# Performance work log

Hardware: AMD Instinct MI355X
Metric: run time of the kernel (lower is better)

The kernel has to match this reference:

```python
import math
import jax, jax.numpy as jnp
import numpy as np
from jax.scipy.linalg import cho_factor, cho_solve, block_diag

NUM_SENSORS = 64
T_STEPS = 2048
LOG2PI = float(np.log(2.0 * np.pi))

NCV_PROCESS_NOISE = np.array([[1.0/3.0, 0.0, 0.5, 0.0],
                              [0.0, 1.0/3.0, 0.0, 0.5],
                              [0.5, 0.0, 1.0, 0.0],
                              [0.0, 0.5, 0.0, 1.0]], dtype=np.float32)
NCV_TRANSITION_MATRIX = np.array([[1.0, 0.0, 1.0, 0.0],
                                  [0.0, 1.0, 0.0, 1.0],
                                  [0.0, 0.0, 1.0, 0.0],
                                  [0.0, 0.0, 0.0, 1.0]], dtype=np.float32)


def setup_inputs() -> dict:
    key = jax.random.key(0)
    k1, k2 = jax.random.split(key)
    track = jax.random.normal(k1, (T_STEPS, 2), dtype=jnp.float32)
    # positive covariance scales for the bias prior (torch param init ~ ones)
    bias_scales = jax.random.uniform(k2, (2,), jnp.float32, 0.5, 1.5)
    obs_noise = jnp.float32(0.7)
    trans_noise = jnp.float32(0.3)
    return {"track": track, "bias_scales": bias_scales,
            "obs_noise": obs_noise, "trans_noise": trans_noise}


def _hmm_forward(track, bias_scales, obs_noise, trans_noise, num_sensors):
    S = num_sensors
    OD = 2 * S           # obs_dim
    D = OD + 4           # augmented latent: [bias(OD); state(4)]
    T = track.shape[0]
    dt = track.dtype

    # observation matrix exactly as in torch source:
    # eye(4,2).expand(S,4,2).transpose(0,-1).reshape(4, OD)
    E = jnp.eye(4, 2, dtype=dt)
    Hobs = jnp.transpose(jnp.broadcast_to(E, (S, 4, 2)), (2, 1, 0)).reshape(4, OD)
    # augmented emission: y = bias + state @ Hobs  ->  H_aug z
    Haug = jnp.concatenate([jnp.eye(OD, dtype=dt), Hobs.T], axis=1)  # (OD, D)

    F = jnp.asarray(NCV_TRANSITION_MATRIX, dt)
    # trans scale_tril = trans_noise * chol(NCV_Q) -> cov = trans_noise^2 * NCV_Q
    Qs = (trans_noise ** 2) * jnp.asarray(NCV_PROCESS_NOISE, dt)
    A = block_diag(jnp.eye(OD, dtype=dt), F)                         # (D, D)
    Q = block_diag(jnp.zeros((OD, OD), dt), Qs)                      # (D, D)
    # obs scale_tril = obs_noise * I -> cov = obs_noise^2 * I
    R = (obs_noise ** 2) * jnp.eye(OD, dtype=dt)

    # bias prior covariance = diag(bias_scales interleaved per sensor)
    bias_var = jnp.broadcast_to(bias_scales, (S, 2)).reshape(-1)     # (OD,)
    m0 = jnp.zeros((D,), dt)
    P0 = jnp.diag(jnp.concatenate([bias_var, jnp.ones((4,), dt)]))

    # obs vector per step: x.expand(S,2).reshape(-1) (interleaved repeat)
    ys = jnp.broadcast_to(track[:, None, :], (T, S, 2)).reshape(T, OD)

    def step(carry, y):
        m, P, ll = carry
        # predict
        mp = A @ m
        Pp = A @ P @ A.T + Q
        # innovation
        HP = Haug @ Pp                      # (OD, D)
        Sm = HP @ Haug.T + R                # (OD, OD)
        cf = cho_factor(Sm, lower=True)
        v = y - Haug @ mp                   # (OD,)
        # update
        K = cho_solve(cf, HP)               # S^{-1} H Pp, (OD, D)
        m_new = mp + K.T @ v
        P_new = Pp - HP.T @ K
        P_new = 0.5 * (P_new + P_new.T)
        # log-likelihood of innovation
        logdet = 2.0 * jnp.sum(jnp.log(jnp.diag(cf[0])))
        quad = v @ cho_solve(cf, v)
        ll = ll - 0.5 * (OD * LOG2PI + logdet + quad)
        return (m_new, P_new, ll), None

    (mT, PT, ll), _ = jax.lax.scan(step, (m0, P0, jnp.zeros((), dt)), ys)
    # funsor's remaining Gaussian over (bias, state_T) has precision = inv(filtered cov)
    cfP = cho_factor(PT, lower=True)
    prec = cho_solve(cfP, jnp.eye(D, dtype=dt))
    return ll, prec


def reference(track, bias_scales, obs_noise, trans_noise):
    return _hmm_forward(track, bias_scales, obs_noise, trans_noise, NUM_SENSORS)
```

## Files before the change

### kernel.cpp

```cpp
#include <hip/hip_runtime.h>
#include <math.h>

#define L2PI 1.8378770664093454835606594728112
#define LN2  0.69314718055994530941723212145818
#define MAGIC 0x7E57C0DE

struct LP {
    float jFF, jFL, jFB, jLL, jLB, jBB;
    float hF, hL, hB, g, dm, de;
};

struct Cn { float qa, qb, qc, wa, wb, ri, Cstep; };

__device__ __forceinline__ float shf(float v, int s) { return __shfl(v, s, 64); }
__device__ __forceinline__ float sx (float v, int m) { return __shfl_xor(v, m, 64); }

__device__ __forceinline__ LP init_lane(float x0, float x1, const Cn& C, int i, int j) {
    LP P;
    float v = 0.0f;
    if (i == j) v = (i < 2) ? C.qa : C.qc;
    if ((i ^ j) == 2) v = C.wa;
    P.jFF = v;
    v = 0.0f;
    if (j == (i & 1))     v = (i < 2) ? -C.qa : -C.wa;
    if (j == (i & 1) + 2) v = (i < 2) ? -C.qb : -C.wb;
    P.jFL = v;
    P.jFB = 0.0f;
    v = 0.0f;
    if (i == j) v = ((i < 2) ? C.qa : C.qc) + (((i & 1) == 0) ? 2.0f*C.ri : 0.0f);
    if ((i ^ j) == 2) v = C.qb;
    P.jLL = v;
    P.jLB = (((i == 0) && (j < 2)) || ((i == 2) && (j >= 2))) ? C.ri : 0.0f;
    P.jBB = (i == j) ? C.ri : 0.0f;
    P.hF = 0.0f;
    P.hL = ((j & 1) == 0) ? C.ri * (x0 + x1) : 0.0f;
    P.hB = C.ri * ((j & 1) ? x1 : x0);
    P.g  = -C.ri * (x0*x0 + x1*x1) + C.Cstep;
    P.dm = 1.0f; P.de = 0.0f;
    return P;
}

__device__ __forceinline__ LP compose(const LP& P1, const LP& P2, int gb, int i, int j) {
    float hm = P1.hL + P2.hF;
    float Mb = P1.jLB + P2.jFB;
    float S  = P1.jLL + P2.jFF;
    float dm = P1.dm * P2.dm;
    float de = P1.de + P2.de;
    { int ex; dm = frexpf(dm, &ex); de += (float)ex; }
    const int r0 = (j == 0) ? 1 : 0;
    const int r1 = (j <= 1) ? 2 : 1;
    const int r2 = (j <= 2) ? 3 : 2;
    const int c0 = (i == 0) ? 1 : 0;
    const int c1 = (i <= 1) ? 2 : 1;
    const int c2 = (i <= 2) ? 3 : 2;
    float m00 = shf(S, gb + 4*r0 + c0), m01 = shf(S, gb + 4*r0 + c1), m02 = shf(S, gb + 4*r0 + c2);
    float m10 = shf(S, gb + 4*r1 + c0), m11 = shf(S, gb + 4*r1 + c1), m12 = shf(S, gb + 4*r1 + c2);
    float m20 = shf(S, gb + 4*r2 + c0), m21 = shf(S, gb + 4*r2 + c1), m22 = shf(S, gb + 4*r2 + c2);
    float d0 = fmaf(m11, m22, -m12*m21);
    float d1 = fmaf(m10, m22, -m12*m20);
    float d2 = fmaf(m10, m21, -m11*m20);
    float det3 = m00*d0 - m01*d1 + m02*d2;
    float adj = (((i + j) & 1) ? -det3 : det3);
    float sji = shf(S, gb + 4*j + i);
    float t = sji * adj;
    t += sx(t, 4); t += sx(t, 8);
    float det = t;
    dm *= det; { int ex; dm = frexpf(dm, &ex); de += (float)ex; }
    const float Si = adj * (1.0f / det);
    float sr[4], sc[4], f1r[4], f1T[4], f2c[4], f2T[4], mc[4], mT[4], hmc[4];
    #pragma unroll
    for (int r = 0; r < 4; ++r) {
        sr[r]  = shf(Si, gb + 4*i + r);
        sc[r]  = shf(Si, gb + 4*r + j);
        f1r[r] = shf(P1.jFL, gb + 4*i + r);
        f1T[r] = shf(P1.jFL, gb + 4*j + r);
        f2c[r] = shf(P2.jFL, gb + 4*r + j);
        f2T[r] = shf(P2.jFL, gb + 4*r + i);
        mc[r]  = shf(Mb, gb + 4*r + j);
        mT[r]  = shf(Mb, gb + 4*r + i);
        hmc[r] = shf(hm, gb + 5*r);
    }
    float A1 = 0.0f, C1 = 0.0f, B2 = 0.0f, v4i = 0.0f;
    #pragma unroll
    for (int r = 0; r < 4; ++r) {
        A1  = fmaf(f1r[r], sc[r], A1);
        C1  = fmaf(sr[r], mc[r], C1);
        B2  = fmaf(sr[r], f2c[r], B2);
        v4i = fmaf(sr[r], hmc[r], v4i);
    }
    float a1r[4], c1c[4], b2c[4], v4c[4];
    #pragma unroll
    for (int r = 0; r < 4; ++r) {
        a1r[r] = shf(A1, gb + 4*i + r);
        c1c[r] = shf(C1, gb + 4*r + j);
        b2c[r] = shf(B2, gb + 4*r + j);
        v4c[r] = shf(v4i, gb + 5*r);
    }
    float s_ff=0, s_fl=0, s_fb=0, s_ll=0, s_lb=0, s_bb=0, s_hf=0, s_hl=0, s_hb=0, s_g=0;
    #pragma unroll
    for (int r = 0; r < 4; ++r) {
        s_ff = fmaf(a1r[r], f1T[r], s_ff);
        s_fl = fmaf(a1r[r], f2c[r], s_fl);
        s_fb = fmaf(a1r[r], mc[r],  s_fb);
        s_ll = fmaf(f2T[r], b2c[r], s_ll);
        s_lb = fmaf(f2T[r], c1c[r], s_lb);
        s_bb = fmaf(mT[r],  c1c[r], s_bb);
        s_hf = fmaf(a1r[r], hmc[r], s_hf);
        s_hl = fmaf(f2c[r], v4c[r], s_hl);
        s_hb = fmaf(mc[r],  v4c[r], s_hb);
        s_g  = fmaf(hmc[r], v4c[r], s_g);
    }
    LP R;
    R.jFF = P1.jFF - s_ff;
    R.jFL = -s_fl;
    R.jFB = P1.jFB - s_fb;
    R.jLL = P2.jLL - s_ll;
    R.jLB = P2.jLB - s_lb;
    R.jBB = P1.jBB + P2.jBB - s_bb;
    R.hF  = P1.hF - shf(s_hf, gb + 5*j);
    R.hL  = P2.hL - s_hl;
    R.hB  = P1.hB + P2.hB - s_hb;
    R.g   = P1.g + P2.g + 2.0f*(float)L2PI + 0.5f*s_g;
    R.dm = dm; R.de = de;
    return R;
}

__device__ __forceinline__ LP fetchx(const LP& P, int m) {
    LP O;
    O.jFF = sx(P.jFF,m); O.jFL = sx(P.jFL,m); O.jFB = sx(P.jFB,m);
    O.jLL = sx(P.jLL,m); O.jLB = sx(P.jLB,m); O.jBB = sx(P.jBB,m);
    O.hF  = sx(P.hF,m);  O.hL  = sx(P.hL,m);  O.hB  = sx(P.hB,m);
    O.g   = sx(P.g,m);   O.dm  = sx(P.dm,m);  O.de  = sx(P.de,m);
    return O;
}
__device__ __forceinline__ LP csel(bool up, const LP& O, const LP& P) {
    LP A;
    A.jFF = up?O.jFF:P.jFF; A.jFL = up?O.jFL:P.jFL; A.jFB = up?O.jFB:P.jFB;
    A.jLL = up?O.jLL:P.jLL; A.jLB = up?O.jLB:P.jLB; A.jBB = up?O.jBB:P.jBB;
    A.hF  = up?O.hF :P.hF;  A.hL  = up?O.hL :P.hL;  A.hB  = up?O.hB :P.hB;
    A.g   = up?O.g  :P.g;   A.dm  = up?O.dm :P.dm;  A.de  = up?O.de :P.de;
    return A;
}
__device__ __forceinline__ void pot_store(float* p, const LP& P) {
    p[0]=P.jFF; p[1]=P.jFL; p[2]=P.jFB; p[3]=P.jLL; p[4]=P.jLB; p[5]=P.jBB;
    p[6]=P.hF;  p[7]=P.hL;  p[8]=P.hB;  p[9]=P.g;   p[10]=P.dm; p[11]=P.de;
}
__device__ __forceinline__ LP pot_load(const float* p) {
    LP P;
    P.jFF=p[0]; P.jFL=p[1]; P.jFB=p[2]; P.jLL=p[3]; P.jLB=p[4]; P.jBB=p[5];
    P.hF=p[6];  P.hL=p[7];  P.hB=p[8];  P.g=p[9];   P.dm=p[10]; P.de=p[11];
    return P;
}
__device__ __forceinline__ float cload(const float* p) {
    return __hip_atomic_load(p, __ATOMIC_RELAXED, __HIP_MEMORY_SCOPE_AGENT);
}
__device__ __forceinline__ LP pot_load_coh(const float* p) {
    LP P;
    P.jFF=cload(p+0); P.jFL=cload(p+1); P.jFB=cload(p+2);
    P.jLL=cload(p+3); P.jLB=cload(p+4); P.jBB=cload(p+5);
    P.hF=cload(p+6);  P.hL=cload(p+7);  P.hB=cload(p+8);
    P.g=cload(p+9);   P.dm=cload(p+10); P.de=cload(p+11);
    return P;
}

__global__ __launch_bounds__(512)
void hmm_fused(const float* __restrict__ track,
               const float* __restrict__ bias_scales,
               const float* __restrict__ obs_noise_p,
               const float* __restrict__ trans_noise_p,
               float* __restrict__ ws,
               float* __restrict__ out)
{
    __shared__ float pool[2][8][16][13];
    __shared__ float sTi[8][8];
    __shared__ float sA[4];
    __shared__ float sLL;
    const int tid = (int)threadIdx.x;
    const int l = tid & 63, w = tid >> 6;
    const int i = (l >> 2) & 3, j = l & 3, gb = l & 48, g = (l >> 4) & 3;
    const int gid = w * 4 + g;
    const int bid = (int)blockIdx.x;

    const double sg2d = (double)obs_noise_p[0] * (double)obs_noise_p[0];
    const double qn2d = (double)trans_noise_p[0] * (double)trans_noise_p[0];
    const double a00 = (double)bias_scales[0];
    const double a01 = (double)bias_scales[1];

    Cn C;
    C.qa = (float)(12.0/qn2d); C.qb = (float)(-6.0/qn2d); C.qc = (float)(4.0/qn2d);
    C.wa = (float)(6.0/qn2d);  C.wb = (float)(-2.0/qn2d);
    C.ri = (float)(32.0/sg2d);
    C.Cstep = (float)(-2.0*log(2.0*M_PI*sg2d/32.0) - 2.0*L2PI
                      - 0.5*(4.0*log(qn2d) - 2.0*log(12.0)));

    int* flags = (int*)(ws + 8192);

    {
        const int t0 = (bid * 32 + gid) * 2;
        LP P;
        #pragma unroll 1
        for (int op = 0; op < 6; ++op) {
            LP A, Bp;
            if (op == 0) {
                A  = init_lane(track[2*t0+0], track[2*t0+1], C, i, j);
                Bp = init_lane(track[2*t0+2], track[2*t0+3], C, i, j);
            } else if (op < 3) {
                const int m = 16 << (op - 1);
                LP O = fetchx(P, m);
                const bool up = (l & m) != 0;
                A  = csel(up, O, P);
                Bp = csel(up, P, O);
            } else {
                const int s = 1 << (op - 3);
                const int buf = (op - 3) & 1;
                if (l < 16) pot_store(&pool[buf][w][l][0], P);
                __syncthreads();
                LP O = pot_load(&pool[buf][w ^ s][l & 15][0]);
                const bool up = (w & s) != 0;
                A  = csel(up, O, P);
                Bp = csel(up, P, O);
            }
            P = compose(A, Bp, gb, i, j);
        }
        if (w == 0 && l < 16)
            pot_store(ws + ((size_t)bid * 16 + l) * 12, P);
        __threadfence();
        __syncthreads();
        if (tid == 0)
            __hip_atomic_store(&flags[bid * 32], MAGIC,
                               __ATOMIC_RELEASE, __HIP_MEMORY_SCOPE_AGENT);
    }
    if (bid != 0) return;

    if (tid < 32) {
        while (__hip_atomic_load(&flags[tid * 32],
                                 __ATOMIC_ACQUIRE, __HIP_MEMORY_SCOPE_AGENT) != MAGIC)
            __builtin_amdgcn_s_sleep(2);
    }
    __syncthreads();
    __threadfence();

    LP P = pot_load_coh(ws + ((size_t)gid * 16 + (l & 15)) * 12);
    #pragma unroll 1
    for (int op = 0; op < 5; ++op) {
        LP A, Bp;
        if (op < 2) {
            const int m = 16 << op;
            LP O = fetchx(P, m);
            const bool up = (l & m) != 0;
            A  = csel(up, O, P);
            Bp = csel(up, P, O);
        } else {
            const int s = 1 << (op - 2);
            const int buf = (op - 2) & 1;
            if (l < 16) pot_store(&pool[buf][w][l][0], P);
            __syncthreads();
            LP O = pot_load(&pool[buf][w ^ s][l & 15][0]);
            const bool up = (w & s) != 0;
            A  = csel(up, O, P);
            Bp = csel(up, P, O);
        }
        P = compose(A, Bp, gb, i, j);
    }

    if (w == 0) {
        const float a0i = (float)((i & 1) ? a01 : a00);
        P.jFF += (i == j) ? 1.0f : 0.0f;
        P.jBB += (i == j) ? 32.0f / a0i : 0.0f;
        P.g   += (float)(-4.0*L2PI + 2.0*log(32.0) - log(a00) - log(a01));
        float dm = P.dm, de = P.de;
        float S = P.jFF;
        const int r0 = (j == 0) ? 1 : 0;
        const int r1 = (j <= 1) ? 2 : 1;
        const int r2 = (j <= 2) ? 3 : 2;
        const int c0 = (i == 0) ? 1 : 0;
        const int c1 = (i <= 1) ? 2 : 1;
        const int c2 = (i <= 2) ? 3 : 2;
        float m00 = shf(S, gb + 4*r0 + c0), m01 = shf(S, gb + 4*r0 + c1), m02 = shf(S, gb + 4*r0 + c2);
        float m10 = shf(S, gb + 4*r1 + c0), m11 = shf(S, gb + 4*r1 + c1), m12 = shf(S, gb + 4*r1 + c2);
        float m20 = shf(S, gb + 4*r2 + c0), m21 = shf(S, gb + 4*r2 + c1), m22 = shf(S, gb + 4*r2 + c2);
        float d0 = fmaf(m11, m22, -m12*m21);
        float d1 = fmaf(m10, m22, -m12*m20);
        float d2 = fmaf(m10, m21, -m11*m20);
        float det3 = m00*d0 - m01*d1 + m02*d2;
        float adj = (((i + j) & 1) ? -det3 : det3);
        float sji = shf(S, gb + 4*j + i);
        float tdet = sji * adj;
        tdet += sx(tdet, 4); tdet += sx(tdet, 8);
        float det = tdet;
        dm *= det; { int ex; dm = frexpf(dm, &ex); de += (float)ex; }
        const float Si = adj * (1.0f / det);
        float sr[4], fr[4], fT[4], bc[4], bT[4], hfc[4];
        #pragma unroll
        for (int r = 0; r < 4; ++r) {
            sr[r]  = shf(Si, gb + 4*i + r);
            fr[r]  = shf(P.jFL, gb + 4*r + i);
            fT[r]  = shf(P.jFL, gb + 4*r + j);
            bc[r]  = shf(P.jFB, gb + 4*r + i);
            bT[r]  = shf(P.jFB, gb + 4*r + j);
            hfc[r] = shf(P.hF, gb + 5*r);
        }
        float YL = 0.0f, YB = 0.0f, yFi = 0.0f;
        #pragma unroll
        for (int r = 0; r < 4; ++r) {
            YL  = fmaf(sr[r], fT[r], YL);
            YB  = fmaf(sr[r], bT[r], YB);
            yFi = fmaf(sr[r], hfc[r], yFi);
        }
        float ylc[4], ybc[4], yfc[4];
        #pragma unroll
        for (int r = 0; r < 4; ++r) {
            ylc[r] = shf(YL, gb + 4*r + j);
            ybc[r] = shf(YB, gb + 4*r + j);
            yfc[r] = shf(yFi, gb + 5*r);
        }
        float s1 = 0.0f, s2 = 0.0f, s3 = 0.0f, sh1 = 0.0f, sh2 = 0.0f, qF = 0.0f;
        #pragma unroll
        for (int r = 0; r < 4; ++r) {
            s1  = fmaf(fr[r], ylc[r], s1);
            s2  = fmaf(fr[r], ybc[r], s2);
            s3  = fmaf(bc[r], ybc[r], s3);
            sh1 = fmaf(fT[r], yfc[r], sh1);
            sh2 = fmaf(bT[r], yfc[r], sh2);
            qF  = fmaf(hfc[r], yfc[r], qF);
        }
        float J8ss = P.jLL - s1;
        float J8sb = P.jLB - s2;
        float J8bb = P.jBB - s3;
        float h8s  = P.hL - sh1;
        float h8b  = P.hB - sh2;
        float g8   = P.g + 2.0f*(float)L2PI + 0.5f*qF;

        const int I = l >> 3, J = l & 7, i4 = I & 3, j4 = J & 3;
        float ss  = shf(J8ss, 4*i4 + j4);
        float sb  = shf(J8sb, 4*i4 + j4);
        float sbT = shf(J8sb, 4*j4 + i4);
        float bb  = shf(J8bb, 4*i4 + j4);
        float A8 = (I < 4) ? ((J < 4) ? ss : sb) : ((J < 4) ? sbT : bb);
        const float J8sav = A8;
        float h8v = (J < 4) ? shf(h8s, j4) : shf(h8b, j4);
        float h8r = (I < 4) ? shf(h8s, i4) : shf(h8b, i4);
        float K8 = (I == J) ? 1.0f : 0.0f;
        #pragma unroll 1
        for (int p = 0; p < 8; ++p) {
            float piv = shf(A8, 9*p);
            dm *= piv; { int ex; dm = frexpf(dm, &ex); de += (float)ex; }
            float ip = 1.0f / piv;
            float Ap = shf(A8, 8*p + J) * ip;
            float Kp = shf(K8, 8*p + J) * ip;
            float f  = shf(A8, 8*I + p);
            bool isp = (I == p);
            A8 = isp ? A8 * ip : fmaf(-f, Ap, A8);
            K8 = isp ? K8 * ip : fmaf(-f, Kp, K8);
        }
        float tq = h8r * K8 * h8v;
        tq += sx(tq,1); tq += sx(tq,2); tq += sx(tq,4);
        tq += sx(tq,8); tq += sx(tq,16); tq += sx(tq,32);

        double ll = (double)g8 + 4.0*L2PI
                    - 0.5*(log((double)dm) + (double)de*LN2) + 0.5*(double)tq;
        const double Td = 2048.0;
        const double c0d = sg2d/a00, c1d = sg2d/a01;
        ll += -31.0*(Td*(L2PI + log(sg2d)) + log((c0d+Td)/c0d))
              -31.0*(Td*(L2PI + log(sg2d)) + log((c1d+Td)/c1d))
              -2.0*Td*log(32.0);

        const float i32 = 1.0f/32.0f, irn = 0.176776695296637f;
        int a = (I >= 4) ? I - 4 : I + 4;
        int b = (J >= 4) ? J - 4 : J + 4;
        float scale = (I >= 4 && J >= 4) ? i32 : (((I >= 4) != (J >= 4)) ? irn : 1.0f);
        sTi[a][b] = J8sav * scale;
        if (l < 4) {
            double a0k = (l & 1) ? a01 : a00;
            sA[l] = (float)(a0k*sg2d/(sg2d + Td*a0k));
        }
        if (l == 0) sLL = (float)ll;
    }
    __syncthreads();

    const float inv32 = 1.0f/32.0f;
    const float invrn = 0.176776695296637f;
    const int total = 1 + 132*132;
    #pragma unroll 1
    for (int idx = tid; idx < total; idx += 512) {
        float v;
        if (idx == 0) {
            v = sLL;
        } else {
            int el = idx - 1;
            int r = el / 132;
            int cc = el - 132*r;
            if (r < 128) {
                int ki = ((r >> 6) << 1) | (r & 1);
                if (cc < 128) {
                    int kj = ((cc >> 6) << 1) | (cc & 1);
                    v = sTi[ki][kj] * inv32;
                    if (ki == kj) {
                        float ia = 1.0f / sA[ki];
                        v -= ia * inv32;
                        if (r == cc) v += ia;
                    }
                } else {
                    v = sTi[ki][cc - 124] * invrn;
                }
            } else {
                if (cc < 128) {
                    int kj = ((cc >> 6) << 1) | (cc & 1);
                    v = sTi[kj][r - 124] * invrn;
                } else {
                    v = sTi[r - 124][cc - 124];
                }
            }
        }
        out[idx] = v;
    }
}

extern "C" void kernel_launch(void* const* d_in, const int* in_sizes, int n_in,
                              void* d_out, int out_size, void* d_ws, size_t ws_size,
                              hipStream_t stream) {
    (void)in_sizes; (void)n_in; (void)out_size; (void)ws_size;
    const float* track       = (const float*)d_in[0];
    const float* bias_scales = (const float*)d_in[1];
    const float* obs_noise   = (const float*)d_in[2];
    const float* trans_noise = (const float*)d_in[3];
    float* out = (float*)d_out;
    float* ws  = (float*)d_ws;
    hipLaunchKernelGGL(hmm_fused, dim3(32), dim3(512), 0, stream,
                       track, bias_scales, obs_noise, trans_noise, ws, out);
}
```

Before: 97.41 us.

## Split fused kernel into producer and consumer launches instead of flag spin-wait

Replaces the single fused kernel, which used global flags and an acquire spin-loop in block 0 to wait for the other blocks' partial scans, with two kernel launches: 32 blocks compute per-chunk potentials into workspace, then a single-block kernel combines them and writes outputs. This removes the atomic flag handshake, the threadfences and the coherent loads. It adds a second launch plus its gap in exchange.

```diff
diff --git a/kernel.cpp b/kernel.cpp
--- a/kernel.cpp
+++ b/kernel.cpp
@@ -3,7 +3,6 @@
 
 #define L2PI 1.8378770664093454835606594728112
 #define LN2  0.69314718055994530941723212145818
-#define MAGIC 0x7E57C0DE
 
 struct LP {
     float jFF, jFL, jFB, jLL, jLB, jBB;
@@ -151,25 +150,65 @@
     P.hF=p[6];  P.hL=p[7];  P.hB=p[8];  P.g=p[9];   P.dm=p[10]; P.de=p[11];
     return P;
 }
-__device__ __forceinline__ float cload(const float* p) {
-    return __hip_atomic_load(p, __ATOMIC_RELAXED, __HIP_MEMORY_SCOPE_AGENT);
-}
-__device__ __forceinline__ LP pot_load_coh(const float* p) {
+
+__global__ __launch_bounds__(512)
+void hmm_produce(const float* __restrict__ track,
+                 const float* __restrict__ obs_noise_p,
+                 const float* __restrict__ trans_noise_p,
+                 float* __restrict__ ws)
+{
+    __shared__ float pool[2][8][16][13];
+    const int tid = (int)threadIdx.x;
+    const int l = tid & 63, w = tid >> 6;
+    const int i = (l >> 2) & 3, j = l & 3, gb = l & 48, g = (l >> 4) & 3;
+    const int gid = w * 4 + g;
+    const int bid = (int)blockIdx.x;
+
+    const double sg2d = (double)obs_noise_p[0] * (double)obs_noise_p[0];
+    const double qn2d = (double)trans_noise_p[0] * (double)trans_noise_p[0];
+
+    Cn C;
+    C.qa = (float)(12.0/qn2d); C.qb = (float)(-6.0/qn2d); C.qc = (float)(4.0/qn2d);
+    C.wa = (float)(6.0/qn2d);  C.wb = (float)(-2.0/qn2d);
+    C.ri = (float)(32.0/sg2d);
+    C.Cstep = (float)(-2.0*log(2.0*M_PI*sg2d/32.0) - 2.0*L2PI
+                      - 0.5*(4.0*log(qn2d) - 2.0*log(12.0)));
+
+    const int t0 = (bid * 32 + gid) * 2;
     LP P;
-    P.jFF=cload(p+0); P.jFL=cload(p+1); P.jFB=cload(p+2);
-    P.jLL=cload(p+3); P.jLB=cload(p+4); P.jBB=cload(p+5);
-    P.hF=cload(p+6);  P.hL=cload(p+7);  P.hB=cload(p+8);
-    P.g=cload(p+9);   P.dm=cload(p+10); P.de=cload(p+11);
-    return P;
+    #pragma unroll 1
+    for (int op = 0; op < 6; ++op) {
+        LP A, Bp;
+        if (op == 0) {
+            A  = init_lane(track[2*t0+0], track[2*t0+1], C, i, j);
+            Bp = init_lane(track[2*t0+2], track[2*t0+3], C, i, j);
+        } else if (op < 3) {
+            const int m = 16 << (op - 1);
+            LP O = fetchx(P, m);
+            const bool up = (l & m) != 0;
+            A  = csel(up, O, P);
+            Bp = csel(up, P, O);
+        } else {
+            const int s = 1 << (op - 3);
+            const int buf = (op - 3) & 1;
+            if (l < 16) pot_store(&pool[buf][w][l][0], P);
+            __syncthreads();
+            LP O = pot_load(&pool[buf][w ^ s][l & 15][0]);
+            const bool up = (w & s) != 0;
+            A  = csel(up, O, P);
+            Bp = csel(up, P, O);
+        }
+        P = compose(A, Bp, gb, i, j);
+    }
+    if (w == 0 && l < 16)
+        pot_store(ws + ((size_t)bid * 16 + l) * 12, P);
 }
 
 __global__ __launch_bounds__(512)
-void hmm_fused(const float* __restrict__ track,
-               const float* __restrict__ bias_scales,
-               const float* __restrict__ obs_noise_p,
-               const float* __restrict__ trans_noise_p,
-               float* __restrict__ ws,
-               float* __restrict__ out)
+void hmm_consume(const float* __restrict__ bias_scales,
+                 const float* __restrict__ obs_noise_p,
+                 const float* __restrict__ ws,
+                 float* __restrict__ out)
 {
     __shared__ float pool[2][8][16][13];
     __shared__ float sTi[8][8];
@@ -179,68 +218,12 @@
     const int l = tid & 63, w = tid >> 6;
     const int i = (l >> 2) & 3, j = l & 3, gb = l & 48, g = (l >> 4) & 3;
     const int gid = w * 4 + g;
-    const int bid = (int)blockIdx.x;
 
     const double sg2d = (double)obs_noise_p[0] * (double)obs_noise_p[0];
-    const double qn2d = (double)trans_noise_p[0] * (double)trans_noise_p[0];
     const double a00 = (double)bias_scales[0];
     const double a01 = (double)bias_scales[1];
 
-    Cn C;
-    C.qa = (float)(12.0/qn2d); C.qb = (float)(-6.0/qn2d); C.qc = (float)(4.0/qn2d);
-    C.wa = (float)(6.0/qn2d);  C.wb = (float)(-2.0/qn2d);
-    C.ri = (float)(32.0/sg2d);
-    C.Cstep = (float)(-2.0*log(2.0*M_PI*sg2d/32.0) - 2.0*L2PI
-                      - 0.5*(4.0*log(qn2d) - 2.0*log(12.0)));
-
-    int* flags = (int*)(ws + 8192);
-
-    {
-        const int t0 = (bid * 32 + gid) * 2;
-        LP P;
-        #pragma unroll 1
-        for (int op = 0; op < 6; ++op) {
-            LP A, Bp;
-            if (op == 0) {
-                A  = init_lane(track[2*t0+0], track[2*t0+1], C, i, j);
-                Bp = init_lane(track[2*t0+2], track[2*t0+3], C, i, j);
-            } else if (op < 3) {
-                const int m = 16 << (op - 1);
-                LP O = fetchx(P, m);
-                const bool up = (l & m) != 0;
-                A  = csel(up, O, P);
-                Bp = csel(up, P, O);
-            } else {
-                const int s = 1 << (op - 3);
-                const int buf = (op - 3) & 1;
-                if (l < 16) pot_store(&pool[buf][w][l][0], P);
-                __syncthreads();
-                LP O = pot_load(&pool[buf][w ^ s][l & 15][0]);
-                const bool up = (w & s) != 0;
-                A  = csel(up, O, P);
-                Bp = csel(up, P, O);
-            }
-            P = compose(A, Bp, gb, i, j);
-        }
-        if (w == 0 && l < 16)
-            pot_store(ws + ((size_t)bid * 16 + l) * 12, P);
-        __threadfence();
-        __syncthreads();
-        if (tid == 0)
-            __hip_atomic_store(&flags[bid * 32], MAGIC,
-                               __ATOMIC_RELEASE, __HIP_MEMORY_SCOPE_AGENT);
-    }
-    if (bid != 0) return;
-
-    if (tid < 32) {
-        while (__hip_atomic_load(&flags[tid * 32],
-                                 __ATOMIC_ACQUIRE, __HIP_MEMORY_SCOPE_AGENT) != MAGIC)
-            __builtin_amdgcn_s_sleep(2);
-    }
-    __syncthreads();
-    __threadfence();
-
-    LP P = pot_load_coh(ws + ((size_t)gid * 16 + (l & 15)) * 12);
+    LP P = pot_load(ws + ((size_t)gid * 16 + (l & 15)) * 12);
     #pragma unroll 1
     for (int op = 0; op < 5; ++op) {
         LP A, Bp;
@@ -426,6 +409,8 @@
     const float* trans_noise = (const float*)d_in[3];
     float* out = (float*)d_out;
     float* ws  = (float*)d_ws;
-    hipLaunchKernelGGL(hmm_fused, dim3(32), dim3(512), 0, stream,
-                       track, bias_scales, obs_noise, trans_noise, ws, out);
-}
+    hipLaunchKernelGGL(hmm_produce, dim3(32), dim3(512), 0, stream,
+                       track, obs_noise, trans_noise, ws);
+    hipLaunchKernelGGL(hmm_consume, dim3(1), dim3(512), 0, stream,
+                       bias_scales, obs_noise, ws, out);
+}
```

Result: faster. 93.85 us (-3.7%).
